# Kernel optimization log

Hardware: AMD Instinct MI355X
Metric: run time of the kernel (lower is better)

Reference implementation:

```python
import jax, jax.numpy as jnp
import numpy as np

N_NODES = 100000
N_EDGES = 1250000
IN_CH = 64
HID_CH = 128
OUT_CH = 128


def setup_inputs() -> dict:
    key = jax.random.key(0)
    ks = jax.random.split(key, 8)
    x = jax.random.normal(ks[0], (N_NODES, IN_CH), dtype=jnp.float32)
    edge_index = jax.random.randint(ks[1], (2, N_EDGES), 0, N_NODES, dtype=jnp.int64)
    # SAGEConv params: lin_l (applied to mean-aggregated neighbors, has bias),
    # lin_r (applied to root/self features, no bias). Glorot-ish scale.
    s1 = 1.0 / np.sqrt(IN_CH)
    s2 = 1.0 / np.sqrt(HID_CH)
    W1l = jax.random.normal(ks[2], (IN_CH, HID_CH), dtype=jnp.float32) * s1
    b1 = jnp.zeros((HID_CH,), dtype=jnp.float32)
    W1r = jax.random.normal(ks[3], (IN_CH, HID_CH), dtype=jnp.float32) * s1
    W2l = jax.random.normal(ks[4], (HID_CH, OUT_CH), dtype=jnp.float32) * s2
    b2 = jnp.zeros((OUT_CH,), dtype=jnp.float32)
    W2r = jax.random.normal(ks[5], (HID_CH, OUT_CH), dtype=jnp.float32) * s2
    return {"x": x, "edge_index": edge_index, "W1l": W1l, "b1": b1, "W1r": W1r,
            "W2l": W2l, "b2": b2, "W2r": W2r}


def _sage_conv(x, src, dst, Wl, b, Wr, n_nodes):
    # mean aggregation of neighbor features (PyG SAGEConv default aggr='mean')
    msg = x[src]                                            # [E, d] gather
    agg = jax.ops.segment_sum(msg, dst, num_segments=n_nodes)   # [N, d]
    cnt = jax.ops.segment_sum(jnp.ones((src.shape[0],), x.dtype), dst,
                              num_segments=n_nodes)         # [N]
    mean = agg / jnp.maximum(cnt, 1.0)[:, None]             # 0 for isolated nodes
    return mean @ Wl + b + x @ Wr                           # lin_l(aggr) + lin_r(x)


def reference(x, edge_index, W1l, b1, W1r, W2l, b2, W2r):
    src, dst = edge_index[0], edge_index[1]
    n = x.shape[0]
    h = jax.nn.relu(_sage_conv(x, src, dst, W1l, b1, W1r, n))
    # dropout is identity in eval mode
    out = _sage_conv(h, src, dst, W2l, b2, W2r, n)
    return out
```

## Files before the change

### kernel.cpp

```cpp
#include <hip/hip_runtime.h>

typedef __attribute__((ext_vector_type(8))) short bf16x8;
typedef __attribute__((ext_vector_type(4))) float f32x4;
typedef __attribute__((ext_vector_type(2))) float f32x2;

#define BCAP 8192
#define EPB  4096


__device__ __forceinline__ void split_bf16(float a, short& hi, short& lo) {
    union { float f; unsigned u; } ua; ua.f = a;
    unsigned hb = ua.u & 0xFFFF0000u;
    hi = (short)(hb >> 16);
    union { unsigned u; float f; } uh; uh.u = hb;
    float r = a - uh.f;
    union { float f; unsigned u; } ur; ur.f = r;
    unsigned rb = ur.u + 0x7FFFu + ((ur.u >> 16) & 1u);
    lo = (short)(rb >> 16);
}

__device__ __forceinline__ unsigned short f2bf_rne(float f) {
    union { float f; unsigned u; } a; a.f = f;
    unsigned r = a.u + 0x7FFFu + ((a.u >> 16) & 1u);
    return (unsigned short)(r >> 16);
}

__device__ __forceinline__ float bf_lo(unsigned v) {
    union { unsigned u; float f; } c; c.u = v << 16; return c.f;
}
__device__ __forceinline__ float bf_hi(unsigned v) {
    union { unsigned u; float f; } c; c.u = v & 0xFFFF0000u; return c.f;
}
__device__ __forceinline__ f32x2 bf_unpack2(unsigned v) {
    f32x2 r; r.x = bf_lo(v); r.y = bf_hi(v); return r;
}


__global__ void k_prep(const float* __restrict__ W1l, const float* __restrict__ W1r,
                       const float* __restrict__ W2l, const float* __restrict__ W2r,
                       short* __restrict__ b1hi, short* __restrict__ b1lo,
                       short* __restrict__ b2hi, short* __restrict__ b2lo,
                       int* __restrict__ bcursor, int NB) {
    int t = blockIdx.x * blockDim.x + threadIdx.x;
    if (t < NB) bcursor[t] = t * BCAP;
    const float* W; short *Bh, *Bl; int kcbase, idx;
    if (t < 8192)       { W = W1l; Bh = b1hi; Bl = b1lo; kcbase = 0; idx = t; }
    else if (t < 16384) { W = W1r; Bh = b1hi; Bl = b1lo; kcbase = 2; idx = t - 8192; }
    else if (t < 32768) { W = W2l; Bh = b2hi; Bl = b2lo; kcbase = 0; idx = t - 16384; }
    else if (t < 49152) { W = W2r; Bh = b2hi; Bl = b2lo; kcbase = 4; idx = t - 32768; }
    else return;
    int k = idx >> 7, c = idx & 127;
    short h, l;
    split_bf16(W[idx], h, l);
    int kq = kcbase * 32 + k;
    int dst = (((kq >> 5) * 8 + (c >> 4)) * 64 + ((kq & 31) >> 3) * 16 + (c & 15)) * 8 + (kq & 7);
    Bh[dst] = h;
    Bl[dst] = l;
}


__global__ void k_xcast(const float* __restrict__ x, int n4,
                        unsigned long long* __restrict__ x16) {
    int i = blockIdx.x * blockDim.x + threadIdx.x;
    if (i >= n4) return;
    float4 v = ((const float4*)x)[i];
    unsigned long long p = (unsigned long long)f2bf_rne(v.x)
                         | ((unsigned long long)f2bf_rne(v.y) << 16)
                         | ((unsigned long long)f2bf_rne(v.z) << 32)
                         | ((unsigned long long)f2bf_rne(v.w) << 48);
    x16[i] = p;
}


__global__ __launch_bounds__(256)
void k_bscatter(const int* __restrict__ src, const int* __restrict__ dst, int E, int NB,
                int* __restrict__ bcursor, int* __restrict__ bedges) {
    __shared__ int hist[512];
    __shared__ int base[512];
    const int t = threadIdx.x;
    const int e0 = blockIdx.x * EPB;
    for (int b = t; b < NB; b += 256) hist[b] = 0;
    __syncthreads();
    for (int i = t; i < EPB; i += 256) {
        int e = e0 + i;
        if (e < E) atomicAdd(&hist[dst[e] >> 9], 1);
    }
    __syncthreads();
    for (int b = t; b < NB; b += 256) {
        int c = hist[b];
        base[b] = c ? atomicAdd(&bcursor[b], c) : 0;
        hist[b] = 0;
    }
    __syncthreads();
    for (int i = t; i < EPB; i += 256) {
        int e = e0 + i;
        if (e < E) {
            int d = dst[e];
            int b = d >> 9;
            int pos = base[b] + atomicAdd(&hist[b], 1);
            if (pos < (b + 1) * BCAP)
                bedges[pos] = (src[e] << 9) | (d & 511);
        }
    }
}

__global__ void k_bscan(const int* __restrict__ bcursor, int NB,
                        int* __restrict__ bbase, int* __restrict__ offsets, int N) {
    __shared__ int sd[256];
    const int t = threadIdx.x;
    int c = 0;
    if (t < NB) {
        c = bcursor[t] - t * BCAP;
        if (c > BCAP) c = BCAP;
    }
    sd[t] = c;
    __syncthreads();
    for (int off = 1; off < 256; off <<= 1) {
        int tv = (t >= off) ? sd[t - off] : 0;
        __syncthreads();
        sd[t] += tv;
        __syncthreads();
    }
    int incl = sd[t];
    if (t < NB) bbase[t] = incl - c;
    if (t == 255) {
        bbase[NB] = sd[255];
        offsets[N] = sd[255];
    }
}

__global__ __launch_bounds__(256)
void k_bsort(const int* __restrict__ bedges, const int* __restrict__ bcursor,
             const int* __restrict__ bbase, int N,
             int* __restrict__ offsets, int* __restrict__ ssrc) {
    __shared__ int cnt[512];
    __shared__ int cur[512];
    __shared__ int sc[256];
    const int t = threadIdx.x;
    const int b = blockIdx.x;
    const int node0 = b << 9;
    const int nn = min(512, N - node0);
    int ecount = bcursor[b] - b * BCAP;
    if (ecount > BCAP) ecount = BCAP;
    const int ebase = b * BCAP;
    const int obase = bbase[b];

    cnt[t] = 0; cnt[t + 256] = 0;
    __syncthreads();
    for (int i = t; i < ecount; i += 256)
        atomicAdd(&cnt[bedges[ebase + i] & 511], 1);
    __syncthreads();

    int v0 = cnt[t];
    sc[t] = v0;
    __syncthreads();
    for (int off = 1; off < 256; off <<= 1) {
        int tv = (t >= off) ? sc[t - off] : 0;
        __syncthreads();
        sc[t] += tv;
        __syncthreads();
    }
    int excl0 = sc[t] - v0;
    int tot0 = sc[255];
    int v1 = cnt[t + 256];
    __syncthreads();
    sc[t] = v1;
    __syncthreads();
    for (int off = 1; off < 256; off <<= 1) {
        int tv = (t >= off) ? sc[t - off] : 0;
        __syncthreads();
        sc[t] += tv;
        __syncthreads();
    }
    int excl1 = sc[t] - v1 + tot0;

    cur[t] = obase + excl0;
    cur[t + 256] = obase + excl1;
    if (t < nn) offsets[node0 + t] = obase + excl0;
    if (t + 256 < nn) offsets[node0 + t + 256] = obase + excl1;
    __syncthreads();

    for (int i = t; i < ecount; i += 256) {
        int p = bedges[ebase + i];
        int pos = atomicAdd(&cur[p & 511], 1);
        ssrc[pos] = (int)((unsigned)p >> 9);
    }
}


__global__ void k_agg64bf(const unsigned short* __restrict__ feat,
                          const int* __restrict__ offsets,
                          const int* __restrict__ ssrc, int N,
                          unsigned short* __restrict__ mout) {
    const int lane = threadIdx.x & 63;
    const int cl = lane & 31;
    const int wid = threadIdx.x >> 6;
    const int node = (blockIdx.x * (blockDim.x >> 6) + wid) * 2 + (lane >> 5);
    if (node >= N) return;
    const int beg = offsets[node], end = offsets[node + 1];
    f32x2 accA = {0.f, 0.f}, accB = {0.f, 0.f};
    for (int j = beg; j < end; j += 8) {
        int s[8]; bool ok[8];
        #pragma unroll
        for (int u = 0; u < 8; ++u) {
            int jj = j + u;
            ok[u] = jj < end;
            s[u] = ssrc[ok[u] ? jj : end - 1];
        }
        unsigned v[8];
        #pragma unroll
        for (int u = 0; u < 8; ++u) {
            unsigned raw = *(const unsigned*)(feat + (size_t)s[u] * 64 + cl * 2);
            v[u] = ok[u] ? raw : 0u;
        }
        accA += bf_unpack2(v[0]); accB += bf_unpack2(v[1]);
        accA += bf_unpack2(v[2]); accB += bf_unpack2(v[3]);
        accA += bf_unpack2(v[4]); accB += bf_unpack2(v[5]);
        accA += bf_unpack2(v[6]); accB += bf_unpack2(v[7]);
    }
    const float inv = (end > beg) ? 1.f / (float)(end - beg) : 0.f;
    f32x2 m = (accA + accB);
    unsigned packed = (unsigned)f2bf_rne(m.x * inv) | ((unsigned)f2bf_rne(m.y * inv) << 16);
    *(unsigned*)(mout + (size_t)node * 64 + cl * 2) = packed;
}

__global__ void k_agg128bf(const unsigned short* __restrict__ feat,
                           const int* __restrict__ offsets,
                           const int* __restrict__ ssrc, int N,
                           unsigned short* __restrict__ mout) {
    const int lane = threadIdx.x & 63;
    const int cq = lane & 31;
    const int wid = threadIdx.x >> 6;
    const int node = (blockIdx.x * (blockDim.x >> 6) + wid) * 2 + (lane >> 5);
    if (node >= N) return;
    const int beg = offsets[node], end = offsets[node + 1];
    f32x2 a01 = {0.f, 0.f}, a23 = {0.f, 0.f};
    f32x2 b01 = {0.f, 0.f}, b23 = {0.f, 0.f};
    for (int j = beg; j < end; j += 8) {
        int s[8]; bool ok[8];
        #pragma unroll
        for (int u = 0; u < 8; ++u) {
            int jj = j + u;
            ok[u] = jj < end;
            s[u] = ssrc[ok[u] ? jj : end - 1];
        }
        uint2 v[8];
        #pragma unroll
        for (int u = 0; u < 8; ++u) {
            uint2 raw = *(const uint2*)(feat + (size_t)s[u] * 128 + cq * 4);
            v[u].x = ok[u] ? raw.x : 0u;
            v[u].y = ok[u] ? raw.y : 0u;
        }
        a01 += bf_unpack2(v[0].x); a23 += bf_unpack2(v[0].y);
        b01 += bf_unpack2(v[1].x); b23 += bf_unpack2(v[1].y);
        a01 += bf_unpack2(v[2].x); a23 += bf_unpack2(v[2].y);
        b01 += bf_unpack2(v[3].x); b23 += bf_unpack2(v[3].y);
        a01 += bf_unpack2(v[4].x); a23 += bf_unpack2(v[4].y);
        b01 += bf_unpack2(v[5].x); b23 += bf_unpack2(v[5].y);
        a01 += bf_unpack2(v[6].x); a23 += bf_unpack2(v[6].y);
        b01 += bf_unpack2(v[7].x); b23 += bf_unpack2(v[7].y);
    }
    const float inv = (end > beg) ? 1.f / (float)(end - beg) : 0.f;
    f32x2 m01 = (a01 + b01), m23 = (a23 + b23);
    uint2 packed;
    packed.x = (unsigned)f2bf_rne(m01.x * inv) | ((unsigned)f2bf_rne(m01.y * inv) << 16);
    packed.y = (unsigned)f2bf_rne(m23.x * inv) | ((unsigned)f2bf_rne(m23.y * inv) << 16);
    *(uint2*)(mout + (size_t)node * 128 + cq * 4) = packed;
}


template <int KHALF, bool RELU, bool OUT16>
__global__ __launch_bounds__(256, 2)
void k_mgemmbf(const unsigned short* __restrict__ A0, const unsigned short* __restrict__ A1,
               const short* __restrict__ Bhi, const short* __restrict__ Blo,
               const float* __restrict__ bias, void* __restrict__ outp, int M) {
    constexpr int NC = KHALF / 32;
    const int lane = threadIdx.x & 63;
    const int w = threadIdx.x >> 6;
    const int row0 = blockIdx.x * 128 + w * 32;
    const int rfrag = lane & 15;
    const int kg = lane >> 4;

    int r0 = row0 + rfrag;      if (r0 > M - 1) r0 = M - 1;
    int r1 = row0 + 16 + rfrag; if (r1 > M - 1) r1 = M - 1;

    const unsigned short* p00 = A0 + (size_t)r0 * KHALF + kg * 8;
    const unsigned short* p01 = A0 + (size_t)r1 * KHALF + kg * 8;
    const unsigned short* p10 = A1 + (size_t)r0 * KHALF + kg * 8;
    const unsigned short* p11 = A1 + (size_t)r1 * KHALF + kg * 8;

    bf16x8 a[2 * NC][2];
    #pragma unroll
    for (int c = 0; c < NC; ++c) {
        a[c][0]      = *(const bf16x8*)(p00 + c * 32);
        a[c][1]      = *(const bf16x8*)(p01 + c * 32);
        a[NC + c][0] = *(const bf16x8*)(p10 + c * 32);
        a[NC + c][1] = *(const bf16x8*)(p11 + c * 32);
    }

    f32x4 acc[2][8];
    #pragma unroll
    for (int mi = 0; mi < 2; ++mi)
        #pragma unroll
        for (int ni = 0; ni < 8; ++ni) {
            f32x4 z = {0.f, 0.f, 0.f, 0.f};
            acc[mi][ni] = z;
        }

    #pragma unroll
    for (int kc = 0; kc < 2 * NC; ++kc) {
        const short* bhc = Bhi + (size_t)kc * 4096 + (size_t)lane * 8;
        const short* blc = Blo + (size_t)kc * 4096 + (size_t)lane * 8;
        #pragma unroll
        for (int ni = 0; ni < 8; ++ni) {
            bf16x8 bhv = *(const bf16x8*)(bhc + ni * 512);
            bf16x8 blv = *(const bf16x8*)(blc + ni * 512);
            #pragma unroll
            for (int mi = 0; mi < 2; ++mi) {
                acc[mi][ni] = __builtin_amdgcn_mfma_f32_16x16x32_bf16(a[kc][mi], bhv, acc[mi][ni], 0, 0, 0);
                acc[mi][ni] = __builtin_amdgcn_mfma_f32_16x16x32_bf16(a[kc][mi], blv, acc[mi][ni], 0, 0, 0);
            }
        }
    }

    #pragma unroll
    for (int ni = 0; ni < 8; ++ni) {
        const int col = ni * 16 + rfrag;
        const float bv = bias[col];
        #pragma unroll
        for (int mi = 0; mi < 2; ++mi) {
            #pragma unroll
            for (int r = 0; r < 4; ++r) {
                int row = row0 + mi * 16 + kg * 4 + r;
                if (row < M) {
                    float val = acc[mi][ni][r] + bv;
                    if (RELU) val = fmaxf(val, 0.f);
                    if (OUT16)
                        ((unsigned short*)outp)[(size_t)row * 128 + col] = f2bf_rne(val);
                    else
                        ((float*)outp)[(size_t)row * 128 + col] = val;
                }
            }
        }
    }
}


extern "C" void kernel_launch(void* const* d_in, const int* in_sizes, int n_in,
                              void* d_out, int out_size, void* d_ws, size_t ws_size,
                              hipStream_t stream) {
    const float* x   = (const float*)d_in[0];
    const int*   ei  = (const int*)d_in[1];
    const float* W1l = (const float*)d_in[2];
    const float* b1  = (const float*)d_in[3];
    const float* W1r = (const float*)d_in[4];
    const float* W2l = (const float*)d_in[5];
    const float* b2  = (const float*)d_in[6];
    const float* W2r = (const float*)d_in[7];
    float* out = (float*)d_out;

    const int N = in_sizes[0] / 64;
    const int E = in_sizes[1] / 2;
    const int* src = ei;
    const int* dst = ei + E;
    const int NB = (N + 511) >> 9;

    char* ws = (char*)d_ws;
    auto alloc = [&](size_t bytes) -> void* {
        void* p = (void*)ws;
        ws += (bytes + 255) & ~(size_t)255;
        return p;
    };
    int* offsets  = (int*)alloc(4ull * (N + 1));
    int* ssrc     = (int*)alloc(4ull * E);
    unsigned short* h16 = (unsigned short*)alloc(2ull * N * 128);
    unsigned short* R   = (unsigned short*)alloc(2ull * N * 128);
    short* b1hi   = (short*)alloc(2ull * 128 * 128);
    short* b1lo   = (short*)alloc(2ull * 128 * 128);
    short* b2hi   = (short*)alloc(2ull * 256 * 128);
    short* b2lo   = (short*)alloc(2ull * 256 * 128);
    int* bcursor  = (int*)alloc(4ull * (NB + 1));
    int* bbase    = (int*)alloc(4ull * (NB + 1));
    int* bedges = (int*)R;
    unsigned short* mean1_16 = R;
    unsigned short* x16 = R + (size_t)N * 64;
    unsigned short* mean16 = R;

    k_prep<<<192, 256, 0, stream>>>(W1l, W1r, W2l, W2r, b1hi, b1lo, b2hi, b2lo,
                                    bcursor, NB);

    k_bscatter<<<(E + EPB - 1) / EPB, 256, 0, stream>>>(src, dst, E, NB, bcursor, bedges);
    k_bscan<<<1, 256, 0, stream>>>(bcursor, NB, bbase, offsets, N);
    k_bsort<<<NB, 256, 0, stream>>>(bedges, bcursor, bbase, N, offsets, ssrc);

    k_xcast<<<(N * 16 + 255) / 256, 256, 0, stream>>>(x, N * 16, (unsigned long long*)x16);

    const int GB = (N + 127) / 128;
    const int AB = (N + 7) / 8;

    k_agg64bf<<<AB, 256, 0, stream>>>(x16, offsets, ssrc, N, mean1_16);
    k_mgemmbf<64, true, true><<<GB, 256, 0, stream>>>(mean1_16, x16, b1hi, b1lo, b1, h16, N);

    k_agg128bf<<<AB, 256, 0, stream>>>(h16, offsets, ssrc, N, mean16);
    k_mgemmbf<128, false, false><<<GB, 256, 0, stream>>>(mean16, h16, b2hi, b2lo, b2, out, N);
}
```

Before: 274.1 us.

## Remove bucket scan kernel via fixed-stride buckets; stage GEMM weights in LDS

Eliminates the single-block scan kernel. Each bucket's sorted edges go in a fixed BCAP-strided region of ssrc, and each node stores an int2 begin/end pair. The aggregation kernels get an unpredicated 8-wide main loop with a separate masked tail. The GEMM now copies each B weight chunk into shared memory per k-step instead of every wave loading it from global memory, at the cost of extra barriers and removing the kc-loop unroll.

```diff
diff --git a/kernel.cpp b/kernel.cpp
--- a/kernel.cpp
+++ b/kernel.cpp
@@ -104,35 +104,9 @@
     }
 }
 
-__global__ void k_bscan(const int* __restrict__ bcursor, int NB,
-                        int* __restrict__ bbase, int* __restrict__ offsets, int N) {
-    __shared__ int sd[256];
-    const int t = threadIdx.x;
-    int c = 0;
-    if (t < NB) {
-        c = bcursor[t] - t * BCAP;
-        if (c > BCAP) c = BCAP;
-    }
-    sd[t] = c;
-    __syncthreads();
-    for (int off = 1; off < 256; off <<= 1) {
-        int tv = (t >= off) ? sd[t - off] : 0;
-        __syncthreads();
-        sd[t] += tv;
-        __syncthreads();
-    }
-    int incl = sd[t];
-    if (t < NB) bbase[t] = incl - c;
-    if (t == 255) {
-        bbase[NB] = sd[255];
-        offsets[N] = sd[255];
-    }
-}
-
 __global__ __launch_bounds__(256)
-void k_bsort(const int* __restrict__ bedges, const int* __restrict__ bcursor,
-             const int* __restrict__ bbase, int N,
-             int* __restrict__ offsets, int* __restrict__ ssrc) {
+void k_bsort(const int* __restrict__ bedges, const int* __restrict__ bcursor, int N,
+             int2* __restrict__ offs, int* __restrict__ ssrc) {
     __shared__ int cnt[512];
     __shared__ int cur[512];
     __shared__ int sc[256];
@@ -143,7 +117,7 @@
     int ecount = bcursor[b] - b * BCAP;
     if (ecount > BCAP) ecount = BCAP;
     const int ebase = b * BCAP;
-    const int obase = bbase[b];
+    const int obase = b * BCAP;
 
     cnt[t] = 0; cnt[t + 256] = 0;
     __syncthreads();
@@ -176,8 +150,8 @@
 
     cur[t] = obase + excl0;
     cur[t + 256] = obase + excl1;
-    if (t < nn) offsets[node0 + t] = obase + excl0;
-    if (t + 256 < nn) offsets[node0 + t + 256] = obase + excl1;
+    if (t < nn) { int2 o; o.x = obase + excl0; o.y = obase + excl0 + v0; offs[node0 + t] = o; }
+    if (t + 256 < nn) { int2 o; o.x = obase + excl1; o.y = obase + excl1 + v1; offs[node0 + t + 256] = o; }
     __syncthreads();
 
     for (int i = t; i < ecount; i += 256) {
@@ -189,7 +163,7 @@
 
 
 __global__ void k_agg64bf(const unsigned short* __restrict__ feat,
-                          const int* __restrict__ offsets,
+                          const int2* __restrict__ offs,
                           const int* __restrict__ ssrc, int N,
                           unsigned short* __restrict__ mout) {
     const int lane = threadIdx.x & 63;
@@ -197,27 +171,34 @@
     const int wid = threadIdx.x >> 6;
     const int node = (blockIdx.x * (blockDim.x >> 6) + wid) * 2 + (lane >> 5);
     if (node >= N) return;
-    const int beg = offsets[node], end = offsets[node + 1];
+    const int2 be = offs[node];
+    const int beg = be.x, end = be.y;
     f32x2 accA = {0.f, 0.f}, accB = {0.f, 0.f};
-    for (int j = beg; j < end; j += 8) {
-        int s[8]; bool ok[8];
-        #pragma unroll
-        for (int u = 0; u < 8; ++u) {
-            int jj = j + u;
-            ok[u] = jj < end;
-            s[u] = ssrc[ok[u] ? jj : end - 1];
-        }
+    int j = beg;
+    for (; j + 8 <= end; j += 8) {
+        int s[8];
+        #pragma unroll
+        for (int u = 0; u < 8; ++u) s[u] = ssrc[j + u];
         unsigned v[8];
         #pragma unroll
-        for (int u = 0; u < 8; ++u) {
-            unsigned raw = *(const unsigned*)(feat + (size_t)s[u] * 64 + cl * 2);
-            v[u] = ok[u] ? raw : 0u;
-        }
+        for (int u = 0; u < 8; ++u)
+            v[u] = *(const unsigned*)(feat + (size_t)s[u] * 64 + cl * 2);
         accA += bf_unpack2(v[0]); accB += bf_unpack2(v[1]);
         accA += bf_unpack2(v[2]); accB += bf_unpack2(v[3]);
         accA += bf_unpack2(v[4]); accB += bf_unpack2(v[5]);
         accA += bf_unpack2(v[6]); accB += bf_unpack2(v[7]);
     }
+    if (j < end) {
+        #pragma unroll
+        for (int u = 0; u < 8; ++u) {
+            int jj = j + u;
+            bool ok = jj < end;
+            int s = ssrc[ok ? jj : end - 1];
+            unsigned raw = *(const unsigned*)(feat + (size_t)s * 64 + cl * 2);
+            unsigned v = ok ? raw : 0u;
+            if (u & 1) accB += bf_unpack2(v); else accA += bf_unpack2(v);
+        }
+    }
     const float inv = (end > beg) ? 1.f / (float)(end - beg) : 0.f;
     f32x2 m = (accA + accB);
     unsigned packed = (unsigned)f2bf_rne(m.x * inv) | ((unsigned)f2bf_rne(m.y * inv) << 16);
@@ -225,7 +206,7 @@
 }
 
 __global__ void k_agg128bf(const unsigned short* __restrict__ feat,
-                           const int* __restrict__ offsets,
+                           const int2* __restrict__ offs,
                            const int* __restrict__ ssrc, int N,
                            unsigned short* __restrict__ mout) {
     const int lane = threadIdx.x & 63;
@@ -233,24 +214,19 @@
     const int wid = threadIdx.x >> 6;
     const int node = (blockIdx.x * (blockDim.x >> 6) + wid) * 2 + (lane >> 5);
     if (node >= N) return;
-    const int beg = offsets[node], end = offsets[node + 1];
+    const int2 be = offs[node];
+    const int beg = be.x, end = be.y;
     f32x2 a01 = {0.f, 0.f}, a23 = {0.f, 0.f};
     f32x2 b01 = {0.f, 0.f}, b23 = {0.f, 0.f};
-    for (int j = beg; j < end; j += 8) {
-        int s[8]; bool ok[8];
-        #pragma unroll
-        for (int u = 0; u < 8; ++u) {
-            int jj = j + u;
-            ok[u] = jj < end;
-            s[u] = ssrc[ok[u] ? jj : end - 1];
-        }
+    int j = beg;
+    for (; j + 8 <= end; j += 8) {
+        int s[8];
+        #pragma unroll
+        for (int u = 0; u < 8; ++u) s[u] = ssrc[j + u];
         uint2 v[8];
         #pragma unroll
-        for (int u = 0; u < 8; ++u) {
-            uint2 raw = *(const uint2*)(feat + (size_t)s[u] * 128 + cq * 4);
-            v[u].x = ok[u] ? raw.x : 0u;
-            v[u].y = ok[u] ? raw.y : 0u;
-        }
+        for (int u = 0; u < 8; ++u)
+            v[u] = *(const uint2*)(feat + (size_t)s[u] * 128 + cq * 4);
         a01 += bf_unpack2(v[0].x); a23 += bf_unpack2(v[0].y);
         b01 += bf_unpack2(v[1].x); b23 += bf_unpack2(v[1].y);
         a01 += bf_unpack2(v[2].x); a23 += bf_unpack2(v[2].y);
@@ -260,6 +236,19 @@
         a01 += bf_unpack2(v[6].x); a23 += bf_unpack2(v[6].y);
         b01 += bf_unpack2(v[7].x); b23 += bf_unpack2(v[7].y);
     }
+    if (j < end) {
+        #pragma unroll
+        for (int u = 0; u < 8; ++u) {
+            int jj = j + u;
+            bool ok = jj < end;
+            int s = ssrc[ok ? jj : end - 1];
+            uint2 raw = *(const uint2*)(feat + (size_t)s * 128 + cq * 4);
+            unsigned vx = ok ? raw.x : 0u;
+            unsigned vy = ok ? raw.y : 0u;
+            if (u & 1) { b01 += bf_unpack2(vx); b23 += bf_unpack2(vy); }
+            else       { a01 += bf_unpack2(vx); a23 += bf_unpack2(vy); }
+        }
+    }
     const float inv = (end > beg) ? 1.f / (float)(end - beg) : 0.f;
     f32x2 m01 = (a01 + b01), m23 = (a23 + b23);
     uint2 packed;
@@ -275,8 +264,11 @@
                const short* __restrict__ Bhi, const short* __restrict__ Blo,
                const float* __restrict__ bias, void* __restrict__ outp, int M) {
     constexpr int NC = KHALF / 32;
-    const int lane = threadIdx.x & 63;
-    const int w = threadIdx.x >> 6;
+    __shared__ short lhi[4096];
+    __shared__ short llo[4096];
+    const int tid = threadIdx.x;
+    const int lane = tid & 63;
+    const int w = tid >> 6;
     const int row0 = blockIdx.x * 128 + w * 32;
     const int rfrag = lane & 15;
     const int kg = lane >> 4;
@@ -307,14 +299,21 @@
             acc[mi][ni] = z;
         }
 
-    #pragma unroll
     for (int kc = 0; kc < 2 * NC; ++kc) {
-        const short* bhc = Bhi + (size_t)kc * 4096 + (size_t)lane * 8;
-        const short* blc = Blo + (size_t)kc * 4096 + (size_t)lane * 8;
+        __syncthreads();
+        {
+            const int4* gh = (const int4*)(Bhi + (size_t)kc * 4096);
+            const int4* gl = (const int4*)(Blo + (size_t)kc * 4096);
+            int4* sh = (int4*)lhi;
+            int4* sl = (int4*)llo;
+            sh[tid] = gh[tid]; sh[tid + 256] = gh[tid + 256];
+            sl[tid] = gl[tid]; sl[tid + 256] = gl[tid + 256];
+        }
+        __syncthreads();
         #pragma unroll
         for (int ni = 0; ni < 8; ++ni) {
-            bf16x8 bhv = *(const bf16x8*)(bhc + ni * 512);
-            bf16x8 blv = *(const bf16x8*)(blc + ni * 512);
+            bf16x8 bhv = *(const bf16x8*)(lhi + ni * 512 + lane * 8);
+            bf16x8 blv = *(const bf16x8*)(llo + ni * 512 + lane * 8);
             #pragma unroll
             for (int mi = 0; mi < 2; ++mi) {
                 acc[mi][ni] = __builtin_amdgcn_mfma_f32_16x16x32_bf16(a[kc][mi], bhv, acc[mi][ni], 0, 0, 0);
@@ -371,8 +370,8 @@
         ws += (bytes + 255) & ~(size_t)255;
         return p;
     };
-    int* offsets  = (int*)alloc(4ull * (N + 1));
-    int* ssrc     = (int*)alloc(4ull * E);
+    int2* offs    = (int2*)alloc(8ull * N);
+    int* ssrc     = (int*)alloc(4ull * NB * BCAP);
     unsigned short* h16 = (unsigned short*)alloc(2ull * N * 128);
     unsigned short* R   = (unsigned short*)alloc(2ull * N * 128);
     short* b1hi   = (short*)alloc(2ull * 128 * 128);
@@ -380,7 +379,6 @@
     short* b2hi   = (short*)alloc(2ull * 256 * 128);
     short* b2lo   = (short*)alloc(2ull * 256 * 128);
     int* bcursor  = (int*)alloc(4ull * (NB + 1));
-    int* bbase    = (int*)alloc(4ull * (NB + 1));
     int* bedges = (int*)R;
     unsigned short* mean1_16 = R;
     unsigned short* x16 = R + (size_t)N * 64;
@@ -390,17 +388,16 @@
                                     bcursor, NB);
 
     k_bscatter<<<(E + EPB - 1) / EPB, 256, 0, stream>>>(src, dst, E, NB, bcursor, bedges);
-    k_bscan<<<1, 256, 0, stream>>>(bcursor, NB, bbase, offsets, N);
-    k_bsort<<<NB, 256, 0, stream>>>(bedges, bcursor, bbase, N, offsets, ssrc);
+    k_bsort<<<NB, 256, 0, stream>>>(bedges, bcursor, N, offs, ssrc);
 
     k_xcast<<<(N * 16 + 255) / 256, 256, 0, stream>>>(x, N * 16, (unsigned long long*)x16);
 
     const int GB = (N + 127) / 128;
     const int AB = (N + 7) / 8;
 
-    k_agg64bf<<<AB, 256, 0, stream>>>(x16, offsets, ssrc, N, mean1_16);
+    k_agg64bf<<<AB, 256, 0, stream>>>(x16, offs, ssrc, N, mean1_16);
     k_mgemmbf<64, true, true><<<GB, 256, 0, stream>>>(mean1_16, x16, b1hi, b1lo, b1, h16, N);
 
-    k_agg128bf<<<AB, 256, 0, stream>>>(h16, offsets, ssrc, N, mean16);
+    k_agg128bf<<<AB, 256, 0, stream>>>(h16, offs, ssrc, N, mean16);
     k_mgemmbf<128, false, false><<<GB, 256, 0, stream>>>(mean16, h16, b2hi, b2lo, b2, out, N);
 }
```

New measurement: 271.8 us. Within noise of the previous version (-0.8%).
